# Kernel optimization log

Hardware: AMD Instinct MI355X
Metric: run time of the kernel (lower is better)

The kernel has to match this reference:

```python
import jax, jax.numpy as jnp
import numpy as np

B, N, F_IN, F_OUT = 8, 2048, 256, 256


def setup_inputs() -> dict:
    key = jax.random.key(0)
    k1, k2, k3, k4 = jax.random.split(key, 4)
    x = jax.random.normal(k1, (B, N, F_IN), dtype=jnp.float32)
    adj = jax.random.uniform(k2, (B, N, N), dtype=jnp.float32)
    W = jax.random.normal(k3, (F_IN, F_OUT), dtype=jnp.float32) * (1.0 / np.sqrt(F_IN))
    b = jax.random.normal(k4, (F_OUT,), dtype=jnp.float32)
    return {"x": x, "adj": adj, "W": W, "b": b}


def reference(x, adj, W, b):
    # GCN with dense adjacency: A_hat = A + I (fill_value=1.0, improved=False)
    n = adj.shape[-1]
    adj = adj + jnp.eye(n, dtype=adj.dtype)[None, :, :]
    deg = adj.sum(axis=-1)                       # [B, N]
    deg_inv_sqrt = deg ** -0.5
    deg_inv_sqrt = jnp.where(jnp.isinf(deg_inv_sqrt), 0.0, deg_inv_sqrt)
    # D^{-1/2} A D^{-1/2} via row/col broadcast (same math as diag bmm)
    adj_norm = deg_inv_sqrt[:, :, None] * adj * deg_inv_sqrt[:, None, :]
    h = jnp.einsum('bnf,fo->bno', x, W)          # linear, no bias
    out = jnp.einsum('bnm,bmo->bno', adj_norm, h)
    return out + b
```

## Files before the change

kernel.cpp:

```cpp
#include <hip/hip_runtime.h>
#include <hip/hip_bf16.h>

#define BB 8
#define NN 2048
#define FF 256
#define NT (NN / 64)

typedef __attribute__((ext_vector_type(8))) short short8;
typedef __attribute__((ext_vector_type(4))) short short4v;
typedef __attribute__((ext_vector_type(4))) float f32x4;
typedef __hip_bfloat16 bf16;

__device__ inline short f2bf(float x) {
  unsigned u = __builtin_bit_cast(unsigned, x);
  unsigned r = (u + 0x7fffu + ((u >> 16) & 1u)) >> 16;
  return (short)r;
}

__device__ inline void gl2lds16(const void* g, void* l) {
  __builtin_amdgcn_global_load_lds((const __attribute__((address_space(1))) void*)g,
                                   (__attribute__((address_space(3))) void*)l, 16, 0, 0);
}

__global__ __launch_bounds__(256)
void degconv_wt_kernel(const float* __restrict__ adj, const float* __restrict__ W,
                       float* __restrict__ dis, bf16* __restrict__ WT,
                       bf16* __restrict__ adjBF) {
  if (blockIdx.x >= BB * NN / 4) {
    int t2 = (blockIdx.x - BB * NN / 4) * 256 + threadIdx.x;
    int k = t2 >> 6, oc = (t2 & 63) * 4;
    float4 v = *reinterpret_cast<const float4*>(W + (size_t)k * FF + oc);
    *reinterpret_cast<short*>(WT + (size_t)(oc + 0) * FF + k) = f2bf(v.x);
    *reinterpret_cast<short*>(WT + (size_t)(oc + 1) * FF + k) = f2bf(v.y);
    *reinterpret_cast<short*>(WT + (size_t)(oc + 2) * FF + k) = f2bf(v.z);
    *reinterpret_cast<short*>(WT + (size_t)(oc + 3) * FF + k) = f2bf(v.w);
    return;
  }
  int wid = threadIdx.x >> 6, lane = threadIdx.x & 63;
  int row = blockIdx.x * 4 + wid;
  const float4* a4 = reinterpret_cast<const float4*>(adj + (size_t)row * NN);
  float4 v[8];
  float s = 0.f;
#pragma unroll
  for (int i = 0; i < 4; i++) {
    v[2 * i]     = a4[i * 128 + 2 * lane];
    v[2 * i + 1] = a4[i * 128 + 2 * lane + 1];
    s += v[2*i].x + v[2*i].y + v[2*i].z + v[2*i].w
       + v[2*i+1].x + v[2*i+1].y + v[2*i+1].z + v[2*i+1].w;
  }
#pragma unroll
  for (int off = 1; off < 64; off <<= 1) s += __shfl_xor(s, off, 64);
  float d = rsqrtf(s + 1.0f);
  if (lane == 0) dis[row] = d;
  int rb = row & (NN - 1);
#pragma unroll
  for (int i = 0; i < 8; i++) {
    int dd = rb - ((i >> 1) * 512 + 8 * lane + 4 * (i & 1));
    v[i].x += (dd == 0) ? 1.0f : 0.0f;
    v[i].y += (dd == 1) ? 1.0f : 0.0f;
    v[i].z += (dd == 2) ? 1.0f : 0.0f;
    v[i].w += (dd == 3) ? 1.0f : 0.0f;
  }
  bf16* orow = adjBF + (size_t)row * NN;
#pragma unroll
  for (int i = 0; i < 4; i++) {
    short8 w;
    w[0] = f2bf(v[2*i].x * d);   w[1] = f2bf(v[2*i].y * d);
    w[2] = f2bf(v[2*i].z * d);   w[3] = f2bf(v[2*i].w * d);
    w[4] = f2bf(v[2*i+1].x * d); w[5] = f2bf(v[2*i+1].y * d);
    w[6] = f2bf(v[2*i+1].z * d); w[7] = f2bf(v[2*i+1].w * d);
    *reinterpret_cast<short8*>(orow + i * 512 + 8 * lane) = w;
  }
}

__global__ __launch_bounds__(256)
void gemm1_kernel(const float* __restrict__ x, const bf16* __restrict__ WT,
                  const float* __restrict__ dis, bf16* __restrict__ gT) {
  __shared__ bf16 lA[128][40];
  __shared__ bf16 lB[128][40];
  int bid = blockIdx.x;
  int mtile = bid & 127, otile = bid >> 7;
  int m0 = mtile * 128, o0 = otile * 128;
  int t = threadIdx.x, wid = t >> 6, lane = t & 63;
  int wr = wid >> 1, wc = wid & 1;
  int srow = t >> 1, sseg = t & 1;
  const int r16 = lane & 15, kb = lane >> 4;

  f32x4 acc[4][4];
#pragma unroll
  for (int i = 0; i < 4; i++)
#pragma unroll
    for (int j = 0; j < 4; j++) acc[i][j] = (f32x4){0.f, 0.f, 0.f, 0.f};

  for (int k0 = 0; k0 < FF; k0 += 32) {
    {
      const float4* ap = reinterpret_cast<const float4*>(
          x + (size_t)(m0 + srow) * FF + k0 + sseg * 16);
      float arr[16];
      float4 v0 = ap[0], v1 = ap[1], v2 = ap[2], v3 = ap[3];
      arr[0]=v0.x; arr[1]=v0.y; arr[2]=v0.z; arr[3]=v0.w;
      arr[4]=v1.x; arr[5]=v1.y; arr[6]=v1.z; arr[7]=v1.w;
      arr[8]=v2.x; arr[9]=v2.y; arr[10]=v2.z; arr[11]=v2.w;
      arr[12]=v3.x; arr[13]=v3.y; arr[14]=v3.z; arr[15]=v3.w;
      short8 w0, w1;
#pragma unroll
      for (int e = 0; e < 8; e++) { w0[e] = f2bf(arr[e]); w1[e] = f2bf(arr[8 + e]); }
      *reinterpret_cast<short8*>(&lA[srow][sseg * 16]) = w0;
      *reinterpret_cast<short8*>(&lA[srow][sseg * 16 + 8]) = w1;
    }
    {
      const short8* bp = reinterpret_cast<const short8*>(
          WT + (size_t)(o0 + srow) * FF + k0 + sseg * 16);
      *reinterpret_cast<short8*>(&lB[srow][sseg * 16]) = bp[0];
      *reinterpret_cast<short8*>(&lB[srow][sseg * 16 + 8]) = bp[1];
    }
    __syncthreads();
    short8 af[4], bfr[4];
#pragma unroll
    for (int mf = 0; mf < 4; mf++)
      af[mf] = *reinterpret_cast<const short8*>(&lA[wr * 64 + mf * 16 + r16][kb * 8]);
#pragma unroll
    for (int nf = 0; nf < 4; nf++)
      bfr[nf] = *reinterpret_cast<const short8*>(&lB[wc * 64 + nf * 16 + r16][kb * 8]);
#pragma unroll
    for (int mf = 0; mf < 4; mf++)
#pragma unroll
      for (int nf = 0; nf < 4; nf++)
        acc[mf][nf] = __builtin_amdgcn_mfma_f32_16x16x32_bf16(af[mf], bfr[nf], acc[mf][nf], 0, 0, 0);
    __syncthreads();
  }

  int b = m0 >> 11;
#pragma unroll
  for (int mf = 0; mf < 4; mf++) {
    int mloc = wr * 64 + mf * 16 + (lane >> 4) * 4;
    int mg = m0 + mloc;
    float4 d4 = *reinterpret_cast<const float4*>(dis + mg);
#pragma unroll
    for (int nf = 0; nf < 4; nf++) {
      int o = o0 + wc * 64 + nf * 16 + r16;
      f32x4 v = acc[mf][nf];
      short4v w;
      w[0] = f2bf(v[0] * d4.x); w[1] = f2bf(v[1] * d4.y);
      w[2] = f2bf(v[2] * d4.z); w[3] = f2bf(v[3] * d4.w);
      *reinterpret_cast<short4v*>(gT + ((size_t)b * FF + o) * NN + (mg & (NN - 1))) = w;
    }
  }
}

__global__ __launch_bounds__(256, 2)
void gemm2_kernel(const bf16* __restrict__ adjBF, const bf16* __restrict__ gT,
                  const float* __restrict__ bias, float* __restrict__ out) {
  __shared__ __align__(16) bf16 lA[2][64 * 64];
  __shared__ __align__(16) bf16 lB[2][128 * 64];
  int bid = blockIdx.x;
  int ob = bid >> 8, g = bid & 255;
  int batch = g >> 5, mtile = g & 31;
  int n0 = mtile * 64, o0 = ob * 128;
  const bf16* Ab = adjBF + ((size_t)batch * NN + n0) * NN;
  const bf16* Bt = gT + ((size_t)batch * FF + o0) * NN;

  int t = threadIdx.x, wid = t >> 6, lane = t & 63;
  int wr = wid >> 1, wc = wid & 1;
  const int r16 = lane & 15, kb = lane >> 4;
  int trow = t >> 3, gslot = (t & 7) ^ (trow & 7);
  const bf16* Ag = Ab + (size_t)trow * NN + 8 * gslot;
  const bf16* Bg = Bt + (size_t)trow * NN + 8 * gslot;

  f32x4 acc[2][4];
#pragma unroll
  for (int i = 0; i < 2; i++)
#pragma unroll
    for (int j = 0; j < 4; j++) acc[i][j] = (f32x4){0.f, 0.f, 0.f, 0.f};

  auto stage = [&](int buf, int ks) {
    bf16* la = &lA[buf][wid * 512];
    bf16* lb = &lB[buf][wid * 512];
#pragma unroll
    for (int q = 0; q < 2; q++)
      gl2lds16(Ag + (size_t)q * 32 * NN + ks * 64, la + q * 2048);
#pragma unroll
    for (int q = 0; q < 4; q++)
      gl2lds16(Bg + (size_t)q * 32 * NN + ks * 64, lb + q * 2048);
  };

  stage(0, 0);
  __syncthreads();
  int cur = 0;
#pragma unroll 1
  for (int ks = 0; ks < NT; ++ks) {
    if (ks + 1 < NT) stage(cur ^ 1, ks + 1);
    const bf16* sa = lA[cur];
    const bf16* sb = lB[cur];
#pragma unroll
    for (int kk = 0; kk < 2; kk++) {
      short8 af[2], bfr[4];
#pragma unroll
      for (int mf = 0; mf < 2; mf++) {
        int ra = wr * 32 + mf * 16 + r16;
        int slot = ((kk << 2) | kb) ^ (ra & 7);
        af[mf] = *reinterpret_cast<const short8*>(&sa[ra * 64 + slot * 8]);
      }
#pragma unroll
      for (int nf = 0; nf < 4; nf++) {
        int rbr = wc * 64 + nf * 16 + r16;
        int slot = ((kk << 2) | kb) ^ (rbr & 7);
        bfr[nf] = *reinterpret_cast<const short8*>(&sb[rbr * 64 + slot * 8]);
      }
#pragma unroll
      for (int mf = 0; mf < 2; mf++)
#pragma unroll
        for (int nf = 0; nf < 4; nf++)
          acc[mf][nf] = __builtin_amdgcn_mfma_f32_16x16x32_bf16(af[mf], bfr[nf], acc[mf][nf], 0, 0, 0);
    }
    __syncthreads();
    cur ^= 1;
  }

  float bv[4];
#pragma unroll
  for (int nf = 0; nf < 4; nf++) bv[nf] = bias[o0 + wc * 64 + nf * 16 + r16];
#pragma unroll
  for (int mf = 0; mf < 2; mf++) {
    int ng = n0 + wr * 32 + mf * 16 + (lane >> 4) * 4;
    float* op0 = out + ((size_t)batch * NN + ng) * FF;
#pragma unroll
    for (int nf = 0; nf < 4; nf++) {
      int o = o0 + wc * 64 + nf * 16 + r16;
      f32x4 v = acc[mf][nf];
      op0[0 * FF + o] = v[0] + bv[nf];
      op0[1 * FF + o] = v[1] + bv[nf];
      op0[2 * FF + o] = v[2] + bv[nf];
      op0[3 * FF + o] = v[3] + bv[nf];
    }
  }
}

extern "C" void kernel_launch(void* const* d_in, const int* in_sizes, int n_in,
                              void* d_out, int out_size, void* d_ws, size_t ws_size,
                              hipStream_t stream) {
  const float* x    = (const float*)d_in[0];
  const float* adj  = (const float*)d_in[1];
  const float* W    = (const float*)d_in[2];
  const float* bias = (const float*)d_in[3];
  float* out = (float*)d_out;

  char* ws = (char*)d_ws;
  float* dis  = (float*)ws;
  bf16* WT    = (bf16*)(ws + (64 << 10));
  bf16* gT    = (bf16*)(ws + (192 << 10));
  bf16* adjBF = (bf16*)(ws + (192 << 10) + (8 << 20));

  degconv_wt_kernel<<<BB * NN / 4 + 64, 256, 0, stream>>>(adj, W, dis, WT, adjBF);
  gemm1_kernel<<<256, 256, 0, stream>>>(x, WT, dis, gT);
  gemm2_kernel<<<512, 256, 0, stream>>>(adjBF, gT, bias, out);
}
```

Baseline: 77.08 us.

## Shrink gemm2 tile to 64x64, double grid, swizzle block order, prioritize MFMA

Cuts the gemm2 output tile from 64x128 to 64x64 and doubles the grid to 1024 blocks, with launch bounds raised to 4 blocks per CU for better occupancy. The block index is remapped so that the four output-column blocks of one adjacency row tile sit close together in launch order, which should help L2 reuse of the adjacency tile. LDS fragments for both k-substeps are loaded before the MFMA burst, and that burst runs under raised wave priority. The smaller tile means the adjacency matrix is read twice as often overall, which raises global and L2 traffic per FLOP.

```diff
diff --git a/kernel.cpp b/kernel.cpp
--- a/kernel.cpp
+++ b/kernel.cpp
@@ -148,40 +148,41 @@
   }
 }
 
-__global__ __launch_bounds__(256, 2)
+__global__ __launch_bounds__(256, 4)
 void gemm2_kernel(const bf16* __restrict__ adjBF, const bf16* __restrict__ gT,
                   const float* __restrict__ bias, float* __restrict__ out) {
   __shared__ __align__(16) bf16 lA[2][64 * 64];
-  __shared__ __align__(16) bf16 lB[2][128 * 64];
+  __shared__ __align__(16) bf16 lB[2][64 * 64];
   int bid = blockIdx.x;
-  int ob = bid >> 8, g = bid & 255;
-  int batch = g >> 5, mtile = g & 31;
-  int n0 = mtile * 64, o0 = ob * 128;
+  int x3 = bid & 7, idx = bid >> 3;
+  int ob = idx & 3, hi = idx >> 2;
+  int gg = hi * 8 + x3;
+  int batch = gg >> 5, mtile = gg & 31;
+  int n0 = mtile * 64, o0 = ob * 64;
   const bf16* Ab = adjBF + ((size_t)batch * NN + n0) * NN;
   const bf16* Bt = gT + ((size_t)batch * FF + o0) * NN;
 
   int t = threadIdx.x, wid = t >> 6, lane = t & 63;
   int wr = wid >> 1, wc = wid & 1;
   const int r16 = lane & 15, kb = lane >> 4;
-  int trow = t >> 3, gslot = (t & 7) ^ (trow & 7);
-  const bf16* Ag = Ab + (size_t)trow * NN + 8 * gslot;
-  const bf16* Bg = Bt + (size_t)trow * NN + 8 * gslot;
-
-  f32x4 acc[2][4];
+  int trow = t >> 3, tslot = t & 7;
+
+  f32x4 acc[2][2];
 #pragma unroll
   for (int i = 0; i < 2; i++)
 #pragma unroll
-    for (int j = 0; j < 4; j++) acc[i][j] = (f32x4){0.f, 0.f, 0.f, 0.f};
+    for (int j = 0; j < 2; j++) acc[i][j] = (f32x4){0.f, 0.f, 0.f, 0.f};
 
   auto stage = [&](int buf, int ks) {
     bf16* la = &lA[buf][wid * 512];
     bf16* lb = &lB[buf][wid * 512];
 #pragma unroll
-    for (int q = 0; q < 2; q++)
-      gl2lds16(Ag + (size_t)q * 32 * NN + ks * 64, la + q * 2048);
-#pragma unroll
-    for (int q = 0; q < 4; q++)
-      gl2lds16(Bg + (size_t)q * 32 * NN + ks * 64, lb + q * 2048);
+    for (int q = 0; q < 2; q++) {
+      int r = q * 32 + trow;
+      int gs = tslot ^ (r & 7);
+      gl2lds16(Ab + (size_t)r * NN + ks * 64 + 8 * gs, la + q * 2048);
+      gl2lds16(Bt + (size_t)r * NN + ks * 64 + 8 * gs, lb + q * 2048);
+    }
   };
 
   stage(0, 0);
@@ -192,41 +193,46 @@
     if (ks + 1 < NT) stage(cur ^ 1, ks + 1);
     const bf16* sa = lA[cur];
     const bf16* sb = lB[cur];
+    short8 af[2][2], bfr[2][2];
 #pragma unroll
     for (int kk = 0; kk < 2; kk++) {
-      short8 af[2], bfr[4];
 #pragma unroll
       for (int mf = 0; mf < 2; mf++) {
         int ra = wr * 32 + mf * 16 + r16;
         int slot = ((kk << 2) | kb) ^ (ra & 7);
-        af[mf] = *reinterpret_cast<const short8*>(&sa[ra * 64 + slot * 8]);
+        af[kk][mf] = *reinterpret_cast<const short8*>(&sa[ra * 64 + slot * 8]);
       }
 #pragma unroll
-      for (int nf = 0; nf < 4; nf++) {
-        int rbr = wc * 64 + nf * 16 + r16;
+      for (int nf = 0; nf < 2; nf++) {
+        int rbr = wc * 32 + nf * 16 + r16;
         int slot = ((kk << 2) | kb) ^ (rbr & 7);
-        bfr[nf] = *reinterpret_cast<const short8*>(&sb[rbr * 64 + slot * 8]);
+        bfr[kk][nf] = *reinterpret_cast<const short8*>(&sb[rbr * 64 + slot * 8]);
       }
+    }
+    __builtin_amdgcn_s_setprio(1);
+#pragma unroll
+    for (int kk = 0; kk < 2; kk++)
 #pragma unroll
       for (int mf = 0; mf < 2; mf++)
 #pragma unroll
-        for (int nf = 0; nf < 4; nf++)
-          acc[mf][nf] = __builtin_amdgcn_mfma_f32_16x16x32_bf16(af[mf], bfr[nf], acc[mf][nf], 0, 0, 0);
-    }
+        for (int nf = 0; nf < 2; nf++)
+          acc[mf][nf] = __builtin_amdgcn_mfma_f32_16x16x32_bf16(
+              af[kk][mf], bfr[kk][nf], acc[mf][nf], 0, 0, 0);
+    __builtin_amdgcn_s_setprio(0);
     __syncthreads();
     cur ^= 1;
   }
 
-  float bv[4];
-#pragma unroll
-  for (int nf = 0; nf < 4; nf++) bv[nf] = bias[o0 + wc * 64 + nf * 16 + r16];
+  float bv[2];
+#pragma unroll
+  for (int nf = 0; nf < 2; nf++) bv[nf] = bias[o0 + wc * 32 + nf * 16 + r16];
 #pragma unroll
   for (int mf = 0; mf < 2; mf++) {
     int ng = n0 + wr * 32 + mf * 16 + (lane >> 4) * 4;
     float* op0 = out + ((size_t)batch * NN + ng) * FF;
 #pragma unroll
-    for (int nf = 0; nf < 4; nf++) {
-      int o = o0 + wc * 64 + nf * 16 + r16;
+    for (int nf = 0; nf < 2; nf++) {
+      int o = o0 + wc * 32 + nf * 16 + r16;
       f32x4 v = acc[mf][nf];
       op0[0 * FF + o] = v[0] + bv[nf];
       op0[1 * FF + o] = v[1] + bv[nf];
@@ -253,5 +259,5 @@
 
   degconv_wt_kernel<<<BB * NN / 4 + 64, 256, 0, stream>>>(adj, W, dis, WT, adjBF);
   gemm1_kernel<<<256, 256, 0, stream>>>(x, WT, dis, gT);
-  gemm2_kernel<<<512, 256, 0, stream>>>(adjBF, gT, bias, out);
-}
+  gemm2_kernel<<<1024, 256, 0, stream>>>(adjBF, gT, bias, out);
+}
```

New measurement: 76.33 us. About the same (-1.0%).

## Use two-wave gemm2 blocks with larger per-wave tiles and MFMA priority

Applied to the files above, without the earlier changes.

Reworks gemm2 from four waves per block, each computing 32x64, to two waves per block, each computing 64x64 of the 64x128 tile. Each wave now reuses more A/B fragments per MFMA and issues fewer LDS reads per flop. The staging loads are reassigned across the smaller thread count, and s_setprio brackets the MFMA burst. The cost is higher register use and fewer waves to hide latency. It also reorders the row-sum in the degree kernel so all loads issue before the reduction.

```diff
diff --git a/kernel.cpp b/kernel.cpp
--- a/kernel.cpp
+++ b/kernel.cpp
@@ -40,14 +40,15 @@
   int row = blockIdx.x * 4 + wid;
   const float4* a4 = reinterpret_cast<const float4*>(adj + (size_t)row * NN);
   float4 v[8];
-  float s = 0.f;
 #pragma unroll
   for (int i = 0; i < 4; i++) {
     v[2 * i]     = a4[i * 128 + 2 * lane];
     v[2 * i + 1] = a4[i * 128 + 2 * lane + 1];
-    s += v[2*i].x + v[2*i].y + v[2*i].z + v[2*i].w
-       + v[2*i+1].x + v[2*i+1].y + v[2*i+1].z + v[2*i+1].w;
-  }
+  }
+  float s = 0.f;
+#pragma unroll
+  for (int i = 0; i < 8; i++)
+    s += v[i].x + v[i].y + v[i].z + v[i].w;
 #pragma unroll
   for (int off = 1; off < 64; off <<= 1) s += __shfl_xor(s, off, 64);
   float d = rsqrtf(s + 1.0f);
@@ -148,7 +149,7 @@
   }
 }
 
-__global__ __launch_bounds__(256, 2)
+__global__ __launch_bounds__(128)
 void gemm2_kernel(const bf16* __restrict__ adjBF, const bf16* __restrict__ gT,
                   const float* __restrict__ bias, float* __restrict__ out) {
   __shared__ __align__(16) bf16 lA[2][64 * 64];
@@ -161,27 +162,30 @@
   const bf16* Bt = gT + ((size_t)batch * FF + o0) * NN;
 
   int t = threadIdx.x, wid = t >> 6, lane = t & 63;
-  int wr = wid >> 1, wc = wid & 1;
   const int r16 = lane & 15, kb = lane >> 4;
-  int trow = t >> 3, gslot = (t & 7) ^ (trow & 7);
-  const bf16* Ag = Ab + (size_t)trow * NN + 8 * gslot;
-  const bf16* Bg = Bt + (size_t)trow * NN + 8 * gslot;
-
-  f32x4 acc[2][4];
-#pragma unroll
-  for (int i = 0; i < 2; i++)
+  int srow = t >> 3, sslot = t & 7;
+
+  f32x4 acc[4][4];
+#pragma unroll
+  for (int i = 0; i < 4; i++)
 #pragma unroll
     for (int j = 0; j < 4; j++) acc[i][j] = (f32x4){0.f, 0.f, 0.f, 0.f};
 
   auto stage = [&](int buf, int ks) {
-    bf16* la = &lA[buf][wid * 512];
-    bf16* lb = &lB[buf][wid * 512];
-#pragma unroll
-    for (int q = 0; q < 2; q++)
-      gl2lds16(Ag + (size_t)q * 32 * NN + ks * 64, la + q * 2048);
-#pragma unroll
-    for (int q = 0; q < 4; q++)
-      gl2lds16(Bg + (size_t)q * 32 * NN + ks * 64, lb + q * 2048);
+#pragma unroll
+    for (int q = 0; q < 4; q++) {
+      int r = q * 16 + srow;
+      int gs = sslot ^ (r & 7);
+      gl2lds16(Ab + (size_t)r * NN + ks * 64 + 8 * gs,
+               &lA[buf][q * 1024 + wid * 512]);
+    }
+#pragma unroll
+    for (int p = 0; p < 8; p++) {
+      int r = p * 16 + srow;
+      int gs = sslot ^ (r & 7);
+      gl2lds16(Bt + (size_t)r * NN + ks * 64 + 8 * gs,
+               &lB[buf][p * 1024 + wid * 512]);
+    }
   };
 
   stage(0, 0);
@@ -194,24 +198,27 @@
     const bf16* sb = lB[cur];
 #pragma unroll
     for (int kk = 0; kk < 2; kk++) {
-      short8 af[2], bfr[4];
-#pragma unroll
-      for (int mf = 0; mf < 2; mf++) {
-        int ra = wr * 32 + mf * 16 + r16;
+      short8 af[4], bfr[4];
+#pragma unroll
+      for (int mf = 0; mf < 4; mf++) {
+        int ra = mf * 16 + r16;
         int slot = ((kk << 2) | kb) ^ (ra & 7);
         af[mf] = *reinterpret_cast<const short8*>(&sa[ra * 64 + slot * 8]);
       }
 #pragma unroll
       for (int nf = 0; nf < 4; nf++) {
-        int rbr = wc * 64 + nf * 16 + r16;
-        int slot = ((kk << 2) | kb) ^ (rbr & 7);
-        bfr[nf] = *reinterpret_cast<const short8*>(&sb[rbr * 64 + slot * 8]);
+        int rb = wid * 64 + nf * 16 + r16;
+        int slot = ((kk << 2) | kb) ^ (rb & 7);
+        bfr[nf] = *reinterpret_cast<const short8*>(&sb[rb * 64 + slot * 8]);
       }
-#pragma unroll
-      for (int mf = 0; mf < 2; mf++)
+      __builtin_amdgcn_s_setprio(1);
+#pragma unroll
+      for (int mf = 0; mf < 4; mf++)
 #pragma unroll
         for (int nf = 0; nf < 4; nf++)
-          acc[mf][nf] = __builtin_amdgcn_mfma_f32_16x16x32_bf16(af[mf], bfr[nf], acc[mf][nf], 0, 0, 0);
+          acc[mf][nf] = __builtin_amdgcn_mfma_f32_16x16x32_bf16(
+              af[mf], bfr[nf], acc[mf][nf], 0, 0, 0);
+      __builtin_amdgcn_s_setprio(0);
     }
     __syncthreads();
     cur ^= 1;
@@ -219,14 +226,14 @@
 
   float bv[4];
 #pragma unroll
-  for (int nf = 0; nf < 4; nf++) bv[nf] = bias[o0 + wc * 64 + nf * 16 + r16];
-#pragma unroll
-  for (int mf = 0; mf < 2; mf++) {
-    int ng = n0 + wr * 32 + mf * 16 + (lane >> 4) * 4;
+  for (int nf = 0; nf < 4; nf++) bv[nf] = bias[o0 + wid * 64 + nf * 16 + r16];
+#pragma unroll
+  for (int mf = 0; mf < 4; mf++) {
+    int ng = n0 + mf * 16 + (lane >> 4) * 4;
     float* op0 = out + ((size_t)batch * NN + ng) * FF;
 #pragma unroll
     for (int nf = 0; nf < 4; nf++) {
-      int o = o0 + wc * 64 + nf * 16 + r16;
+      int o = o0 + wid * 64 + nf * 16 + r16;
       f32x4 v = acc[mf][nf];
       op0[0 * FF + o] = v[0] + bv[nf];
       op0[1 * FF + o] = v[1] + bv[nf];
@@ -253,5 +260,5 @@
 
   degconv_wt_kernel<<<BB * NN / 4 + 64, 256, 0, stream>>>(adj, W, dis, WT, adjBF);
   gemm1_kernel<<<256, 256, 0, stream>>>(x, WT, dis, gT);
-  gemm2_kernel<<<512, 256, 0, stream>>>(adjBF, gT, bias, out);
-}
+  gemm2_kernel<<<512, 128, 0, stream>>>(adjBF, gT, bias, out);
+}
```

Result: slower. 82.15 us (+6.6%).
